# Performance work log

Hardware: AMD Instinct MI355X
Metric: run time of the kernel (lower is better)

## Reference

```python
import jax, jax.numpy as jnp
import numpy as np

N, NFEAT, NHID, NCLASS, H1 = 4096, 512, 64, 16, 8
GAIN = 1.414  # xavier gain used by the torch module
NEG_SLOPE = 0.2
MASK_VAL = -1e10


def _xavier(k, shape):
    fan_in, fan_out = shape[-2], shape[-1]
    lim = GAIN * (6.0 / (fan_in + fan_out)) ** 0.5
    return jax.random.uniform(k, shape, jnp.float32, -lim, lim)


def setup_inputs() -> dict:
    key = jax.random.key(0)
    ks = jax.random.split(key, 10)
    return {
        "x": jax.random.normal(ks[0], (N, NFEAT), jnp.float32),
        "adj": jax.random.randint(ks[1], (N, N), 0, 2, jnp.int32),
        # layer-1 parameters, stacked over H1 heads
        "W1": _xavier(ks[2], (H1, NFEAT, NHID)),
        "b1": jnp.zeros((H1, NHID), jnp.float32),
        "as1": _xavier(ks[3], (H1, NHID, 1))[..., 0],
        "an1": _xavier(ks[4], (H1, NHID, 1))[..., 0],
        # layer-2 parameters (single head, input = H1*NHID due to concat)
        "W2": _xavier(ks[5], (H1 * NHID, NCLASS)),
        "b2": jnp.zeros((NCLASS,), jnp.float32),
        "as2": _xavier(ks[6], (NCLASS, 1))[:, 0],
        "an2": _xavier(ks[7], (NCLASS, 1))[:, 0],
    }


def gat_layer(X, adj_pos, W, b, a_s, a_n):
    # X: [N, Fin], W: [Fin, Fout], a_s/a_n: [Fout], adj_pos: [N, N] bool
    feats = X @ W                                        # [N, Fout]
    s = feats @ a_s                                      # [N]
    nb = feats @ a_n                                     # [N]
    attn = jax.nn.leaky_relu(s[:, None] + nb[None, :], NEG_SLOPE)  # [N, N]
    attn = jnp.where(adj_pos, attn, MASK_VAL)
    attn = jax.nn.softmax(attn, axis=-1)
    # dropout on attn/feats is a no-op in eval mode
    return attn @ feats + b                              # [N, Fout]


def reference(x, adj, W1, b1, as1, an1, W2, b2, as2, an2):
    adj_pos = adj > 0
    # x dropout is a no-op in eval mode
    layer1 = jax.vmap(gat_layer, in_axes=(None, None, 0, 0, 0, 0))
    h = jax.nn.relu(layer1(x, adj_pos, W1, b1, as1, an1))    # [H1, N, NHID]
    h = jnp.transpose(h, (1, 0, 2)).reshape(N, H1 * NHID)    # concat heads on dim 1
    h = jax.nn.elu(h)
    out = jax.nn.relu(gat_layer(h, adj_pos, W2, b2, as2, an2))  # [N, NCLASS]
    return jax.nn.log_softmax(out, axis=1)
```

## Files before the change

kernel.cpp:

```cpp
#include <hip/hip_runtime.h>

#define NN 4096
#define NFEAT 512
#define NHID 64
#define H1 8
#define NCLS 16
#define BND 40.0f
#define VSTR 72
#define FSCL 4096.0f

typedef short bf16x8 __attribute__((ext_vector_type(8)));
typedef _Float16 f16x8 __attribute__((ext_vector_type(8)));
typedef _Float16 h2 __attribute__((ext_vector_type(2)));
typedef __fp16 fp16v2 __attribute__((ext_vector_type(2)));
typedef float f32x4 __attribute__((ext_vector_type(4)));

__device__ __forceinline__ unsigned short f2bf(float f) {
    unsigned u = __float_as_uint(f);
    u += 0x7fffu + ((u >> 16) & 1u);
    return (unsigned short)(u >> 16);
}
__device__ __forceinline__ float leaky(float v) { return fmaxf(v, 0.2f * v); }
__device__ __forceinline__ unsigned pkbf(float lo, float hi) {
    return __builtin_amdgcn_perm(__float_as_uint(hi) + 0x8000u,
                                 __float_as_uint(lo) + 0x8000u, 0x07060302u);
}
__device__ __forceinline__ unsigned pkh(float lo, float hi) {
    union { fp16v2 h; unsigned u; } c;
    c.h = __builtin_amdgcn_cvt_pkrtz(lo, hi);
    return c.u;
}
__device__ __forceinline__ h2 uash(unsigned u) { union { unsigned u; h2 h; } c; c.u = u; return c.h; }
__device__ __forceinline__ unsigned hasu(h2 h) { union { unsigned u; h2 h; } c; c.h = h; return c.u; }
__device__ __forceinline__ bf16x8 mk8(unsigned a, unsigned b, unsigned c, unsigned d) {
    union { unsigned u[4]; bf16x8 v; } cv;
    cv.u[0] = a; cv.u[1] = b; cv.u[2] = c; cv.u[3] = d; return cv.v;
}
__device__ __forceinline__ f16x8 mk8h(unsigned a, unsigned b, unsigned c, unsigned d) {
    union { unsigned u[4]; f16x8 v; } cv;
    cv.u[0] = a; cv.u[1] = b; cv.u[2] = c; cv.u[3] = d; return cv.v;
}

__global__ __launch_bounds__(256)
void k_prep(const int* __restrict__ adj, unsigned long long* __restrict__ bits,
            const float* __restrict__ W1, unsigned short* __restrict__ w1f,
            const float* __restrict__ x, unsigned short* __restrict__ xh)
{
    __shared__ float wt[64][65];
    const int t = threadIdx.x, bx = blockIdx.x;
    if (bx < NN) {
        const int wv = t >> 6, lane = t & 63;
        const int* ap = adj + (size_t)bx * NN;
        for (int w = wv; w < 64; w += 4) {
            unsigned long long m = __ballot(ap[w * 64 + lane] > 0);
            if (lane == 0) bits[(size_t)bx * 64 + w] = m;
        }
        return;
    }
    if (bx >= NN + 64) {
        const int b = bx - NN - 64;
        #pragma unroll
        for (int i = 0; i < 4; ++i) {
            const int f4 = b * 1024 + i * 256 + t;
            const float4 v = ((const float4*)x)[f4];
            uint2 w; w.x = pkh(v.x, v.y); w.y = pkh(v.z, v.w);
            ((uint2*)xh)[f4] = w;
        }
        return;
    }
    const int kt = (bx - NN) & 7, h = (bx - NN) >> 3;
    #pragma unroll
    for (int i = 0; i < 4; ++i) {
        const int f = t + 256 * i;
        const int r = f >> 4, c4 = f & 15;
        const float4 v = *(const float4*)(W1 + ((size_t)(h * NFEAT) + kt * 64 + r) * NHID + c4 * 4);
        wt[r][c4 * 4 + 0] = v.x; wt[r][c4 * 4 + 1] = v.y;
        wt[r][c4 * 4 + 2] = v.z; wt[r][c4 * 4 + 3] = v.w;
    }
    __syncthreads();
    #pragma unroll
    for (int s = 0; s < 2; ++s) {
        const int o = t + s * 256;
        const int kg2 = o >> 8, rem = o & 255;
        const int nt = rem >> 6, lane2 = rem & 63;
        const int qq = lane2 >> 4, nn = lane2 & 15;
        const int kl = kg2 * 32 + qq * 8;
        const int c = nt * 16 + nn;
        uint4 w;
        w.x = pkh(wt[kl + 0][c], wt[kl + 1][c]);
        w.y = pkh(wt[kl + 2][c], wt[kl + 3][c]);
        w.z = pkh(wt[kl + 4][c], wt[kl + 5][c]);
        w.w = pkh(wt[kl + 6][c], wt[kl + 7][c]);
        *(uint4*)(w1f + (((size_t)h * 16 + kt * 2 + kg2) * 4 + nt) * 512 + lane2 * 8) = w;
    }
}

__global__ __launch_bounds__(256)
void k_feats1(const unsigned short* __restrict__ xh, const unsigned short* __restrict__ w1f,
              const float* __restrict__ as1, const float* __restrict__ an1,
              unsigned short* __restrict__ f1bT, float* __restrict__ s1, float* __restrict__ nb1)
{
    const int t = threadIdx.x, wv = t >> 6, lane = t & 63;
    const int q = lane >> 4, n = lane & 15;
    const int h = blockIdx.y, R0 = blockIdx.x * 64;
    const int row = R0 + wv * 16 + n;
    const unsigned short* ap = xh + (size_t)row * NFEAT;
    const unsigned short* wp = w1f + (size_t)h * 16 * 4 * 512 + lane * 8;
    f32x4 acc[4] = {{0.f,0.f,0.f,0.f},{0.f,0.f,0.f,0.f},{0.f,0.f,0.f,0.f},{0.f,0.f,0.f,0.f}};
    #pragma unroll 4
    for (int kg = 0; kg < 16; ++kg) {
        const f16x8 af = *(const f16x8*)(ap + kg * 32 + q * 8);
        #pragma unroll
        for (int nt = 0; nt < 4; ++nt) {
            const f16x8 bf = *(const f16x8*)(wp + (size_t)(kg * 4 + nt) * 512);
            acc[nt] = __builtin_amdgcn_mfma_f32_16x16x32_f16(af, bf, acc[nt], 0, 0, 0);
        }
    }
    #pragma unroll
    for (int nt = 0; nt < 4; ++nt) {
        uint2 w;
        w.x = pkh(acc[nt][0], acc[nt][1]);
        w.y = pkh(acc[nt][2], acc[nt][3]);
        *(uint2*)(f1bT + ((size_t)h * NHID + nt * 16 + n) * NN + R0 + wv * 16 + q * 4) = w;
    }
    float asv[4], anv[4];
    #pragma unroll
    for (int nt = 0; nt < 4; ++nt) {
        asv[nt] = as1[h * NHID + nt * 16 + n];
        anv[nt] = an1[h * NHID + nt * 16 + n];
    }
    #pragma unroll
    for (int i = 0; i < 4; ++i) {
        float ps = acc[0][i]*asv[0] + acc[1][i]*asv[1] + acc[2][i]*asv[2] + acc[3][i]*asv[3];
        float pn = acc[0][i]*anv[0] + acc[1][i]*anv[1] + acc[2][i]*anv[2] + acc[3][i]*anv[3];
        #pragma unroll
        for (int off = 8; off > 0; off >>= 1) {
            ps += __shfl_xor(ps, off, 64);
            pn += __shfl_xor(pn, off, 64);
        }
        if (n == 0) {
            const int idx = R0 + wv * 16 + q * 4 + i;
            s1[h * NN + idx] = ps;
            nb1[h * NN + idx] = pn;
        }
    }
}

__global__ __launch_bounds__(256)
void k_fact1(const float* __restrict__ nb1, unsigned short* __restrict__ F1h,
             unsigned short* __restrict__ F2h, float* __restrict__ nbmax)
{
    const int b = blockIdx.x, t = threadIdx.x;
    const float* p = nb1 + (size_t)b * NN;
    float m = -INFINITY;
    for (int i = t; i < NN; i += 256) m = fmaxf(m, p[i]);
    #pragma unroll
    for (int off = 32; off > 0; off >>= 1) m = fmaxf(m, __shfl_xor(m, off, 64));
    __shared__ float sm[4];
    __shared__ float smx;
    if ((t & 63) == 0) sm[t >> 6] = m;
    __syncthreads();
    if (t == 0) {
        const float mm = fmaxf(fmaxf(sm[0], sm[1]), fmaxf(sm[2], sm[3]));
        smx = mm; nbmax[b] = mm;
    }
    __syncthreads();
    const float mx = smx;
    for (int i = t * 2; i < NN; i += 512) {
        const float d0 = p[i] - mx, d1 = p[i + 1] - mx;
        ((unsigned*)F1h)[((size_t)b * NN + i) >> 1] = pkh(FSCL * __expf(d0), FSCL * __expf(d1));
        ((unsigned*)F2h)[((size_t)b * NN + i) >> 1] = pkh(FSCL * __expf(0.2f * d0), FSCL * __expf(0.2f * d1));
    }
}

__global__ __launch_bounds__(512, 4)
void k_gat1(const unsigned short* __restrict__ f1bT, const float* __restrict__ s1,
            const unsigned short* __restrict__ F1h, const unsigned short* __restrict__ F2h,
            const unsigned long long* __restrict__ abits, const float* __restrict__ b1,
            const float* __restrict__ nbmax1, unsigned short* __restrict__ hcatb)
{
    __shared__ __align__(16) char smem[4 * 2 * 64 * VSTR * 2];
    unsigned short* vT = (unsigned short*)smem;

    const int t = threadIdx.x, wv = t >> 6, lane = t & 63;
    const int q = lane >> 4, n = lane & 15;
    const int rg = wv >> 2, jq = wv & 3;
    const int h = blockIdx.y, R0 = blockIdx.x * 64;
    const int rowA = R0 + rg * 32 + n;
    const int rowB = rowA + 16;
    const float mh = nbmax1[h];
    const float vA = s1[h * NN + rowA] + mh, mhA = leaky(vA);
    const float vB = s1[h * NN + rowB] + mh, mhB = leaky(vB);
    const float E1Af = __expf(vA - mhA), E2Af = __expf(0.2f * vA - mhA);
    const float E1Bf = __expf(vB - mhB), E2Bf = __expf(0.2f * vB - mhB);
    const h2 E1A = {(_Float16)E1Af, (_Float16)E1Af};
    const h2 E2A = {(_Float16)E2Af, (_Float16)E2Af};
    const h2 E1B = {(_Float16)E1Bf, (_Float16)E1Bf};
    const h2 E2B = {(_Float16)E2Bf, (_Float16)E2Bf};
    const unsigned long long* arowA = abits + (size_t)rowA * 64;
    const unsigned long long* arowB = abits + (size_t)rowB * 64;
    const unsigned short* F1p = F1h + (size_t)h * NN;
    const unsigned short* F2p = F2h + (size_t)h * NN;

    const int stile = t >> 7;
    const int sc0 = (t & 127) >> 3, sj8 = t & 7;
    const unsigned short* sbase = f1bT + (size_t)h * NHID * NN + (size_t)sc0 * NN + sj8 * 8;
    const int dof = sc0 * VSTR + sj8 * 8;

    f32x4 accA[4] = {{0.f,0.f,0.f,0.f},{0.f,0.f,0.f,0.f},{0.f,0.f,0.f,0.f},{0.f,0.f,0.f,0.f}};
    f32x4 accB[4] = {{0.f,0.f,0.f,0.f},{0.f,0.f,0.f,0.f},{0.f,0.f,0.f,0.f},{0.f,0.f,0.f,0.f}};
    float lsA = 0.f, lsB = 0.f;

    {
        const int js = stile * 1024;
        int4 v0 = *(const int4*)(sbase + js);
        int4 v1 = *(const int4*)(sbase + (size_t)16 * NN + js);
        int4 v2 = *(const int4*)(sbase + (size_t)32 * NN + js);
        int4 v3 = *(const int4*)(sbase + (size_t)48 * NN + js);
        unsigned short* d = vT + (stile * 2 + 0) * (64 * VSTR) + dof;
        *(int4*)(d) = v0;
        *(int4*)(d + 16 * VSTR) = v1;
        *(int4*)(d + 32 * VSTR) = v2;
        *(int4*)(d + 48 * VSTR) = v3;
    }
    __syncthreads();

    for (int it = 0; it < 16; ++it) {
        const int db = it & 1;
        int4 p0, p1, p2, p3;
        if (it < 15) {
            const int js = stile * 1024 + (it + 1) * 64;
            p0 = *(const int4*)(sbase + js);
            p1 = *(const int4*)(sbase + (size_t)16 * NN + js);
            p2 = *(const int4*)(sbase + (size_t)32 * NN + js);
            p3 = *(const int4*)(sbase + (size_t)48 * NN + js);
        }
        const int j0 = jq * 1024 + it * 64;
        const unsigned long long aA = arowA[j0 >> 6];
        const unsigned long long aB = arowB[j0 >> 6];
        const unsigned short* tbase = vT + (jq * 2 + db) * (64 * VSTR);
        #pragma unroll
        for (int ch = 0; ch < 2; ++ch) {
            const int kb = ch * 32 + q * 8;
            const uint4 f1w = *(const uint4*)(F1p + j0 + kb);
            const uint4 f2w = *(const uint4*)(F2p + j0 + kb);
            const unsigned bA = (unsigned)(aA >> kb) & 0xffu;
            const unsigned bB = (unsigned)(aB >> kb) & 0xffu;
            unsigned uA[4], uB[4];
            h2 sA2 = {(_Float16)0, (_Float16)0};
            h2 sB2 = {(_Float16)0, (_Float16)0};
            #pragma unroll
            for (int jp = 0; jp < 4; ++jp) {
                const h2 f1 = uash(((const unsigned*)&f1w)[jp]);
                const h2 f2 = uash(((const unsigned*)&f2w)[jp]);
                const unsigned mA = ((bA >> (2*jp)) & 1u) * 0x3C00u
                                  + ((bA >> (2*jp+1)) & 1u) * 0x3C000000u;
                const unsigned mB = ((bB >> (2*jp)) & 1u) * 0x3C00u
                                  + ((bB >> (2*jp+1)) & 1u) * 0x3C000000u;
                h2 pA = __builtin_elementwise_max(E1A * f1, E2A * f2) * uash(mA);
                h2 pB = __builtin_elementwise_max(E1B * f1, E2B * f2) * uash(mB);
                sA2 += pA; sB2 += pB;
                uA[jp] = hasu(pA); uB[jp] = hasu(pB);
            }
            lsA += (float)sA2[0] + (float)sA2[1];
            lsB += (float)sB2[0] + (float)sB2[1];
            const f16x8 afA = mk8h(uA[0], uA[1], uA[2], uA[3]);
            const f16x8 afB = mk8h(uB[0], uB[1], uB[2], uB[3]);
            #pragma unroll
            for (int nt = 0; nt < 4; ++nt) {
                const f16x8 bf = *(const f16x8*)(tbase + (nt * 16 + n) * VSTR + kb);
                accA[nt] = __builtin_amdgcn_mfma_f32_16x16x32_f16(afA, bf, accA[nt], 0, 0, 0);
                accB[nt] = __builtin_amdgcn_mfma_f32_16x16x32_f16(afB, bf, accB[nt], 0, 0, 0);
            }
        }
        if (it < 15) {
            unsigned short* d = vT + (stile * 2 + (db ^ 1)) * (64 * VSTR) + dof;
            *(int4*)(d) = p0;
            *(int4*)(d + 16 * VSTR) = p1;
            *(int4*)(d + 32 * VSTR) = p2;
            *(int4*)(d + 48 * VSTR) = p3;
        }
        __syncthreads();
    }

    lsA += __shfl_xor(lsA, 16, 64); lsA += __shfl_xor(lsA, 32, 64);
    lsB += __shfl_xor(lsB, 16, 64); lsB += __shfl_xor(lsB, 32, 64);

    float* cmbf = (float*)smem;
    float* lwf  = (float*)(smem + 69632);
    #pragma unroll
    for (int nt = 0; nt < 4; ++nt)
        #pragma unroll
        for (int i = 0; i < 4; ++i) {
            cmbf[((size_t)jq * 64 + rg * 32 + q * 4 + i) * 68 + nt * 16 + n] = accA[nt][i];
            cmbf[((size_t)jq * 64 + rg * 32 + 16 + q * 4 + i) * 68 + nt * 16 + n] = accB[nt][i];
        }
    if (q == 0) {
        lwf[jq * 64 + rg * 32 + n] = lsA;
        lwf[jq * 64 + rg * 32 + 16 + n] = lsB;
    }
    __syncthreads();

    const int col = t & 63, r8 = t >> 6;
    const float bv = b1[h * NHID + col];
    #pragma unroll
    for (int rr = 0; rr < 8; ++rr) {
        const int r = r8 * 8 + rr;
        float tot = 0.f, lt = 0.f;
        #pragma unroll
        for (int jj = 0; jj < 4; ++jj) {
            tot += cmbf[((size_t)jj * 64 + r) * 68 + col];
            lt  += lwf[jj * 64 + r];
        }
        hcatb[(size_t)(R0 + r) * (H1 * NHID) + h * NHID + col] =
            f2bf(fmaxf(tot / lt + bv, 0.f));
    }
}

__global__ __launch_bounds__(128)
void k_feats2(const unsigned short* __restrict__ hcatb, const float* __restrict__ W2,
              const float* __restrict__ as2, const float* __restrict__ an2,
              unsigned short* __restrict__ f2bT, float* __restrict__ s2,
              float* __restrict__ F1b, float* __restrict__ F2b)
{
    __shared__ __align__(16) unsigned short w2T[NCLS][520];
    const int t = threadIdx.x, wv = t >> 6, lane = t & 63;
    const int q = lane >> 4, n = lane & 15;
    #pragma unroll
    for (int i = 0; i < 16; ++i) {
        const int f4 = t + 128 * i;
        const float4 v = ((const float4*)W2)[f4];
        const int k = f4 >> 2, c0 = (f4 & 3) * 4;
        w2T[c0 + 0][k] = f2bf(v.x); w2T[c0 + 1][k] = f2bf(v.y);
        w2T[c0 + 2][k] = f2bf(v.z); w2T[c0 + 3][k] = f2bf(v.w);
    }
    __syncthreads();

    const int R0 = blockIdx.x * 32;
    const int row = R0 + wv * 16 + n;
    const unsigned short* ap = hcatb + (size_t)row * NFEAT;
    f32x4 acc = {0.f, 0.f, 0.f, 0.f};
    #pragma unroll 4
    for (int k0 = 0; k0 < NFEAT; k0 += 32) {
        const bf16x8 af = *(const bf16x8*)(ap + k0 + q * 8);
        const bf16x8 bf = *(const bf16x8*)&w2T[n][k0 + q * 8];
        acc = __builtin_amdgcn_mfma_f32_16x16x32_bf16(af, bf, acc, 0, 0, 0);
    }
    uint2 w;
    w.x = pkbf(acc[0], acc[1]);
    w.y = pkbf(acc[2], acc[3]);
    *(uint2*)(f2bT + (size_t)n * NN + R0 + wv * 16 + q * 4) = w;
    const float asv = as2[n], anv = an2[n];
    #pragma unroll
    for (int i = 0; i < 4; ++i) {
        float ps = acc[i] * asv, pn = acc[i] * anv;
        #pragma unroll
        for (int off = 8; off > 0; off >>= 1) {
            ps += __shfl_xor(ps, off, 64);
            pn += __shfl_xor(pn, off, 64);
        }
        if (n == 0) {
            const int idx = R0 + wv * 16 + q * 4 + i;
            s2[idx] = ps;
            F1b[idx] = __expf(pn - BND);
            F2b[idx] = __expf(0.2f * (pn - BND));
        }
    }
}

__global__ __launch_bounds__(1024)
void k_gat2(const unsigned short* __restrict__ f2bT, const float* __restrict__ s2,
            const float* __restrict__ F1, const float* __restrict__ F2,
            const unsigned long long* __restrict__ abits, const float* __restrict__ b2,
            float* __restrict__ out)
{
    __shared__ float cmb[16][16][17];
    __shared__ float lw[16][16];
    const int t = threadIdx.x, wv = t >> 6, lane = t & 63;
    const int q = lane >> 4, n = lane & 15;
    const int R0 = blockIdx.x * 16, row = R0 + n;
    const float v = s2[row] + BND, mhat = leaky(v);
    const float E1 = __expf(v - mhat), E2 = __expf(0.2f * v - mhat);
    const unsigned long long* arow = abits + (size_t)row * 64;

    f32x4 acc = {0.f, 0.f, 0.f, 0.f};
    float lsum = 0.f;
    const int jbeg = wv * 256;
    for (int j0 = jbeg; j0 < jbeg + 256; j0 += 64) {
        const unsigned long long a64 = arow[j0 >> 6];
        #pragma unroll
        for (int ch = 0; ch < 2; ++ch) {
            const int kb = ch * 32 + q * 8;
            const float4 f1a = *(const float4*)(F1 + j0 + kb);
            const float4 f1b = *(const float4*)(F1 + j0 + kb + 4);
            const float4 f2a = *(const float4*)(F2 + j0 + kb);
            const float4 f2b = *(const float4*)(F2 + j0 + kb + 4);
            const float F1v[8] = {f1a.x, f1a.y, f1a.z, f1a.w, f1b.x, f1b.y, f1b.z, f1b.w};
            const float F2v[8] = {f2a.x, f2a.y, f2a.z, f2a.w, f2b.x, f2b.y, f2b.z, f2b.w};
            const unsigned b8 = (unsigned)(a64 >> kb) & 0xffu;
            unsigned au[4];
            #pragma unroll
            for (int jp = 0; jp < 4; ++jp) {
                float p0 = fmaxf(E1 * F1v[2*jp],   E2 * F2v[2*jp]);
                float p1 = fmaxf(E1 * F1v[2*jp+1], E2 * F2v[2*jp+1]);
                p0 = ((b8 >> (2*jp)) & 1u) ? p0 : 0.f;
                p1 = ((b8 >> (2*jp+1)) & 1u) ? p1 : 0.f;
                lsum += p0 + p1;
                au[jp] = pkbf(p0, p1);
            }
            const bf16x8 af = mk8(au[0], au[1], au[2], au[3]);
            const bf16x8 bf = *(const bf16x8*)(f2bT + (size_t)n * NN + j0 + kb);
            acc = __builtin_amdgcn_mfma_f32_16x16x32_bf16(af, bf, acc, 0, 0, 0);
        }
    }
    lsum += __shfl_xor(lsum, 16, 64);
    lsum += __shfl_xor(lsum, 32, 64);
    #pragma unroll
    for (int i = 0; i < 4; ++i) cmb[wv][q * 4 + i][n] = acc[i];
    if (q == 0) lw[wv][n] = lsum;
    __syncthreads();

    if (t < 256) {
        const int r = t >> 4, c = t & 15;
        float tot = 0.f, lt = 0.f;
        #pragma unroll
        for (int w16 = 0; w16 < 16; ++w16) { tot += cmb[w16][r][c]; lt += lw[w16][r]; }
        float val = fmaxf(tot / lt + b2[c], 0.f);
        float mx = val;
        #pragma unroll
        for (int off = 1; off < 16; off <<= 1) mx = fmaxf(mx, __shfl_xor(mx, off, 64));
        const float e = __expf(val - mx);
        float se = e;
        #pragma unroll
        for (int off = 1; off < 16; off <<= 1) se += __shfl_xor(se, off, 64);
        out[(size_t)(R0 + r) * NCLS + c] = val - mx - __logf(se);
    }
}

extern "C" void kernel_launch(void* const* d_in, const int* in_sizes, int n_in,
                              void* d_out, int out_size, void* d_ws, size_t ws_size,
                              hipStream_t stream)
{
    const float* x   = (const float*)d_in[0];
    const int*   adj = (const int*)  d_in[1];
    const float* W1  = (const float*)d_in[2];
    const float* b1  = (const float*)d_in[3];
    const float* as1 = (const float*)d_in[4];
    const float* an1 = (const float*)d_in[5];
    const float* W2  = (const float*)d_in[6];
    const float* b2  = (const float*)d_in[7];
    const float* as2 = (const float*)d_in[8];
    const float* an2 = (const float*)d_in[9];
    float* out = (float*)d_out;

    char* ws = (char*)d_ws;
    unsigned long long* abits = (unsigned long long*)(ws);
    unsigned short* f1bT  = (unsigned short*)(ws + (2u << 20));
    unsigned short* xh    = (unsigned short*)(ws + (6u << 20));
    unsigned short* hcatb = xh;
    unsigned short* w1f   = (unsigned short*)(ws + (10u << 20));
    char* ws2 = ws + (10u << 20) + (512u << 10);
    float* s1   = (float*)(ws2);
    float* nb1  = (float*)(ws2 + (128u << 10));
    unsigned short* F1h = (unsigned short*)(ws2 + (256u << 10));
    unsigned short* F2h = (unsigned short*)(ws2 + (320u << 10));
    unsigned short* f2bT = (unsigned short*)(ws2 + (384u << 10));
    float* s2   = (float*)(ws2 + (512u << 10));
    float* F1b  = (float*)(ws2 + (528u << 10));
    float* F2b  = (float*)(ws2 + (544u << 10));
    float* nbmax1 = (float*)(ws2 + (560u << 10));

    k_prep  <<<dim3(NN + 64 + 512), 256, 0, stream>>>(adj, abits, W1, w1f, x, xh);
    k_feats1<<<dim3(NN / 64, H1),   256, 0, stream>>>(xh, w1f, as1, an1, f1bT, s1, nb1);
    k_fact1 <<<dim3(H1),            256, 0, stream>>>(nb1, F1h, F2h, nbmax1);
    k_gat1  <<<dim3(NN / 64, H1),   512, 0, stream>>>(f1bT, s1, F1h, F2h, abits, b1, nbmax1, hcatb);
    k_feats2<<<dim3(NN / 32),       128, 0, stream>>>(hcatb, W2, as2, an2, f2bT, s2, F1b, F2b);
    k_gat2  <<<dim3(NN / 16),       1024, 0, stream>>>(f2bT, s2, F1b, F2b, abits, b2, out);
}
```

Baseline: 212.4 us.

## Fuse neighbor-max into feats1 via atomics, interleave F1/F2, vectorize adj packing

The adjacency bitmask is now packed with int4 loads, each thread producing one byte, over twice as many blocks, replacing the per-wave ballot loop. The per-head max of neighbor scores is computed in k_feats1 with an order-preserving float key and atomicMax, so k_fact1 no longer reduces and runs with many more blocks. F1 and F2 exponent tables are interleaved per 8-element group so k_gat1 reads both from one contiguous region. Grid axes are swapped so heads vary fastest, which changes block scheduling and cache locality, and the atomic key must be zeroed in k_prep before it is used.

```diff
diff --git a/kernel.cpp b/kernel.cpp
--- a/kernel.cpp
+++ b/kernel.cpp
@@ -40,25 +40,41 @@
     union { unsigned u[4]; f16x8 v; } cv;
     cv.u[0] = a; cv.u[1] = b; cv.u[2] = c; cv.u[3] = d; return cv.v;
 }
+__device__ __forceinline__ unsigned fkey(float f) {
+    const unsigned u = __float_as_uint(f);
+    return (u >> 31) ? ~u : (u | 0x80000000u);
+}
+__device__ __forceinline__ float funkey(unsigned k) {
+    return __uint_as_float((k & 0x80000000u) ? (k ^ 0x80000000u) : ~k);
+}
 
 __global__ __launch_bounds__(256)
 void k_prep(const int* __restrict__ adj, unsigned long long* __restrict__ bits,
             const float* __restrict__ W1, unsigned short* __restrict__ w1f,
-            const float* __restrict__ x, unsigned short* __restrict__ xh)
+            const float* __restrict__ x, unsigned short* __restrict__ xh,
+            unsigned* __restrict__ nbkey)
 {
     __shared__ float wt[64][65];
     const int t = threadIdx.x, bx = blockIdx.x;
-    if (bx < NN) {
-        const int wv = t >> 6, lane = t & 63;
-        const int* ap = adj + (size_t)bx * NN;
-        for (int w = wv; w < 64; w += 4) {
-            unsigned long long m = __ballot(ap[w * 64 + lane] > 0);
-            if (lane == 0) bits[(size_t)bx * 64 + w] = m;
-        }
+    if (bx < 2 * NN) {
+        const int row = bx >> 1, half = bx & 1;
+        const int j0 = half * 2048 + t * 8;
+        const int* ap = adj + (size_t)row * NN + j0;
+        const int4 v0 = *(const int4*)(ap);
+        const int4 v1 = *(const int4*)(ap + 4);
+        const unsigned b = (unsigned)(v0.x > 0)        | ((unsigned)(v0.y > 0) << 1)
+                         | ((unsigned)(v0.z > 0) << 2) | ((unsigned)(v0.w > 0) << 3)
+                         | ((unsigned)(v1.x > 0) << 4) | ((unsigned)(v1.y > 0) << 5)
+                         | ((unsigned)(v1.z > 0) << 6) | ((unsigned)(v1.w > 0) << 7);
+        ((unsigned char*)bits)[(size_t)row * 512 + (j0 >> 3)] = (unsigned char)b;
         return;
     }
-    if (bx >= NN + 64) {
-        const int b = bx - NN - 64;
+    if (bx == 2 * NN + 64 + 512) {
+        if (t < H1) nbkey[t] = 0u;
+        return;
+    }
+    if (bx >= 2 * NN + 64) {
+        const int b = bx - (2 * NN + 64);
         #pragma unroll
         for (int i = 0; i < 4; ++i) {
             const int f4 = b * 1024 + i * 256 + t;
@@ -68,7 +84,8 @@
         }
         return;
     }
-    const int kt = (bx - NN) & 7, h = (bx - NN) >> 3;
+    const int idx = bx - 2 * NN;
+    const int kt = idx & 7, h = idx >> 3;
     #pragma unroll
     for (int i = 0; i < 4; ++i) {
         const int f = t + 256 * i;
@@ -98,11 +115,12 @@
 __global__ __launch_bounds__(256)
 void k_feats1(const unsigned short* __restrict__ xh, const unsigned short* __restrict__ w1f,
               const float* __restrict__ as1, const float* __restrict__ an1,
-              unsigned short* __restrict__ f1bT, float* __restrict__ s1, float* __restrict__ nb1)
+              unsigned short* __restrict__ f1bT, float* __restrict__ s1,
+              float* __restrict__ nb1, unsigned* __restrict__ nbkey)
 {
     const int t = threadIdx.x, wv = t >> 6, lane = t & 63;
     const int q = lane >> 4, n = lane & 15;
-    const int h = blockIdx.y, R0 = blockIdx.x * 64;
+    const int h = blockIdx.x, R0 = blockIdx.y * 64;
     const int row = R0 + wv * 16 + n;
     const unsigned short* ap = xh + (size_t)row * NFEAT;
     const unsigned short* wp = w1f + (size_t)h * 16 * 4 * 512 + lane * 8;
@@ -129,6 +147,7 @@
         asv[nt] = as1[h * NHID + nt * 16 + n];
         anv[nt] = an1[h * NHID + nt * 16 + n];
     }
+    float pmax = -1e30f;
     #pragma unroll
     for (int i = 0; i < 4; ++i) {
         float ps = acc[0][i]*asv[0] + acc[1][i]*asv[1] + acc[2][i]*asv[2] + acc[3][i]*asv[3];
@@ -138,46 +157,36 @@
             ps += __shfl_xor(ps, off, 64);
             pn += __shfl_xor(pn, off, 64);
         }
+        pmax = fmaxf(pmax, pn);
         if (n == 0) {
             const int idx = R0 + wv * 16 + q * 4 + i;
             s1[h * NN + idx] = ps;
             nb1[h * NN + idx] = pn;
         }
     }
+    pmax = fmaxf(pmax, __shfl_xor(pmax, 16, 64));
+    pmax = fmaxf(pmax, __shfl_xor(pmax, 32, 64));
+    if (lane == 0) atomicMax(nbkey + h, fkey(pmax));
 }
 
 __global__ __launch_bounds__(256)
-void k_fact1(const float* __restrict__ nb1, unsigned short* __restrict__ F1h,
-             unsigned short* __restrict__ F2h, float* __restrict__ nbmax)
-{
-    const int b = blockIdx.x, t = threadIdx.x;
-    const float* p = nb1 + (size_t)b * NN;
-    float m = -INFINITY;
-    for (int i = t; i < NN; i += 256) m = fmaxf(m, p[i]);
-    #pragma unroll
-    for (int off = 32; off > 0; off >>= 1) m = fmaxf(m, __shfl_xor(m, off, 64));
-    __shared__ float sm[4];
-    __shared__ float smx;
-    if ((t & 63) == 0) sm[t >> 6] = m;
-    __syncthreads();
-    if (t == 0) {
-        const float mm = fmaxf(fmaxf(sm[0], sm[1]), fmaxf(sm[2], sm[3]));
-        smx = mm; nbmax[b] = mm;
-    }
-    __syncthreads();
-    const float mx = smx;
-    for (int i = t * 2; i < NN; i += 512) {
-        const float d0 = p[i] - mx, d1 = p[i + 1] - mx;
-        ((unsigned*)F1h)[((size_t)b * NN + i) >> 1] = pkh(FSCL * __expf(d0), FSCL * __expf(d1));
-        ((unsigned*)F2h)[((size_t)b * NN + i) >> 1] = pkh(FSCL * __expf(0.2f * d0), FSCL * __expf(0.2f * d1));
-    }
+void k_fact1(const float* __restrict__ nb1, const unsigned* __restrict__ nbkey,
+             unsigned short* __restrict__ F12)
+{
+    const int h = blockIdx.x, ck = blockIdx.y, t = threadIdx.x;
+    const float mx = funkey(nbkey[h]);
+    const int j = ck * 512 + t * 2;
+    const float d0 = nb1[h * NN + j] - mx, d1 = nb1[h * NN + j + 1] - mx;
+    unsigned short* base = F12 + ((size_t)h * 512 + (j >> 3)) * 16 + (j & 7);
+    *(unsigned*)(base)     = pkh(FSCL * __expf(d0),        FSCL * __expf(d1));
+    *(unsigned*)(base + 8) = pkh(FSCL * __expf(0.2f * d0), FSCL * __expf(0.2f * d1));
 }
 
 __global__ __launch_bounds__(512, 4)
 void k_gat1(const unsigned short* __restrict__ f1bT, const float* __restrict__ s1,
-            const unsigned short* __restrict__ F1h, const unsigned short* __restrict__ F2h,
-            const unsigned long long* __restrict__ abits, const float* __restrict__ b1,
-            const float* __restrict__ nbmax1, unsigned short* __restrict__ hcatb)
+            const unsigned short* __restrict__ F12, const unsigned long long* __restrict__ abits,
+            const float* __restrict__ b1, const unsigned* __restrict__ nbkey,
+            unsigned short* __restrict__ hcatb)
 {
     __shared__ __align__(16) char smem[4 * 2 * 64 * VSTR * 2];
     unsigned short* vT = (unsigned short*)smem;
@@ -185,10 +194,10 @@
     const int t = threadIdx.x, wv = t >> 6, lane = t & 63;
     const int q = lane >> 4, n = lane & 15;
     const int rg = wv >> 2, jq = wv & 3;
-    const int h = blockIdx.y, R0 = blockIdx.x * 64;
+    const int h = blockIdx.x, R0 = blockIdx.y * 64;
     const int rowA = R0 + rg * 32 + n;
     const int rowB = rowA + 16;
-    const float mh = nbmax1[h];
+    const float mh = funkey(nbkey[h]);
     const float vA = s1[h * NN + rowA] + mh, mhA = leaky(vA);
     const float vB = s1[h * NN + rowB] + mh, mhB = leaky(vB);
     const float E1Af = __expf(vA - mhA), E2Af = __expf(0.2f * vA - mhA);
@@ -199,8 +208,7 @@
     const h2 E2B = {(_Float16)E2Bf, (_Float16)E2Bf};
     const unsigned long long* arowA = abits + (size_t)rowA * 64;
     const unsigned long long* arowB = abits + (size_t)rowB * 64;
-    const unsigned short* F1p = F1h + (size_t)h * NN;
-    const unsigned short* F2p = F2h + (size_t)h * NN;
+    const unsigned short* Fp = F12 + (size_t)h * 512 * 16;
 
     const int stile = t >> 7;
     const int sc0 = (t & 127) >> 3, sj8 = t & 7;
@@ -242,8 +250,9 @@
         #pragma unroll
         for (int ch = 0; ch < 2; ++ch) {
             const int kb = ch * 32 + q * 8;
-            const uint4 f1w = *(const uint4*)(F1p + j0 + kb);
-            const uint4 f2w = *(const uint4*)(F2p + j0 + kb);
+            const unsigned short* fg = Fp + (size_t)((j0 + kb) >> 3) * 16;
+            const uint4 f1w = *(const uint4*)(fg);
+            const uint4 f2w = *(const uint4*)(fg + 8);
             const unsigned bA = (unsigned)(aA >> kb) & 0xffu;
             const unsigned bB = (unsigned)(aB >> kb) & 0xffu;
             unsigned uA[4], uB[4];
@@ -462,18 +471,17 @@
     char* ws2 = ws + (10u << 20) + (512u << 10);
     float* s1   = (float*)(ws2);
     float* nb1  = (float*)(ws2 + (128u << 10));
-    unsigned short* F1h = (unsigned short*)(ws2 + (256u << 10));
-    unsigned short* F2h = (unsigned short*)(ws2 + (320u << 10));
+    unsigned short* F12 = (unsigned short*)(ws2 + (256u << 10));
     unsigned short* f2bT = (unsigned short*)(ws2 + (384u << 10));
     float* s2   = (float*)(ws2 + (512u << 10));
     float* F1b  = (float*)(ws2 + (528u << 10));
     float* F2b  = (float*)(ws2 + (544u << 10));
-    float* nbmax1 = (float*)(ws2 + (560u << 10));
-
-    k_prep  <<<dim3(NN + 64 + 512), 256, 0, stream>>>(adj, abits, W1, w1f, x, xh);
-    k_feats1<<<dim3(NN / 64, H1),   256, 0, stream>>>(xh, w1f, as1, an1, f1bT, s1, nb1);
-    k_fact1 <<<dim3(H1),            256, 0, stream>>>(nb1, F1h, F2h, nbmax1);
-    k_gat1  <<<dim3(NN / 64, H1),   512, 0, stream>>>(f1bT, s1, F1h, F2h, abits, b1, nbmax1, hcatb);
-    k_feats2<<<dim3(NN / 32),       128, 0, stream>>>(hcatb, W2, as2, an2, f2bT, s2, F1b, F2b);
-    k_gat2  <<<dim3(NN / 16),       1024, 0, stream>>>(f2bT, s2, F1b, F2b, abits, b2, out);
-}
+    unsigned* nbkey = (unsigned*)(ws2 + (560u << 10));
+
+    k_prep  <<<dim3(2 * NN + 64 + 512 + 1), 256, 0, stream>>>(adj, abits, W1, w1f, x, xh, nbkey);
+    k_feats1<<<dim3(H1, NN / 64),  256, 0, stream>>>(xh, w1f, as1, an1, f1bT, s1, nb1, nbkey);
+    k_fact1 <<<dim3(H1, 8),        256, 0, stream>>>(nb1, nbkey, F12);
+    k_gat1  <<<dim3(H1, NN / 64),  512, 0, stream>>>(f1bT, s1, F12, abits, b1, nbkey, hcatb);
+    k_feats2<<<dim3(NN / 32),      128, 0, stream>>>(hcatb, W2, as2, an2, f2bT, s2, F1b, F2b);
+    k_gat2  <<<dim3(NN / 16),      1024, 0, stream>>>(f2bT, s2, F1b, F2b, abits, b2, out);
+}
```

New measurement: 220.1 us. +3.7%, slower.
